# Kernel optimization log

Hardware: AMD Instinct MI355X
Metric: run time of the kernel (lower is better)

Reference implementation:

```python
import jax, jax.numpy as jnp
import numpy as np

B, N, D = 8, 2048, 512

def setup_inputs() -> dict:
    key = jax.random.key(0)
    k1, k2, k3, k4 = jax.random.split(key, 4)
    x = jax.random.normal(k1, (B, N, D), dtype=jnp.float32)
    x2 = jax.random.normal(k2, (B, N, D), dtype=jnp.float32)
    # nn.Linear(dim, dim): weight [D, D], bias [D]
    W = jax.random.normal(k3, (D, D), dtype=jnp.float32) * (1.0 / np.sqrt(D))
    b = jax.random.normal(k4, (D,), dtype=jnp.float32) * 0.01
    return {"x": x, "x2": x2, "W": W, "b": b}

def reference(x, x2, W, b):
    # key = softmax(x2.transpose(1,2), dim=1) -> softmax over feature axis D,
    # shape [B, D, N]; equivalently softmax(x2, axis=-1) then transpose.
    key_t = jax.nn.softmax(x2, axis=-1)          # [B, N, D], softmax over D
    query = jax.nn.softmax(x2, axis=1)            # [B, N, D], softmax over N
    # context = value @ key : [B,N,D] @ [B,D,N] -> [B,N,N]
    context = jnp.einsum('bnd,bmd->bnm', x, key_t)
    # atten = context @ query : [B,N,N] @ [B,N,D] -> [B,N,D]
    atten = jnp.einsum('bnm,bmd->bnd', context, query)
    # linear projection: atten @ W.T + b
    return jnp.einsum('bnd,ed->bne', atten, W) + b
```

## Files before the change

### kernel.cpp

```cpp
#include <hip/hip_runtime.h>


typedef __attribute__((ext_vector_type(8))) short          s16x8;
typedef __attribute__((ext_vector_type(8))) unsigned short u16x8;
typedef __attribute__((ext_vector_type(4))) float          f32x4;

#define B_ 8
#define N_ 2048
#define D_ 512

__device__ inline unsigned short f2bf(float f) {
    unsigned u = __float_as_uint(f);
    u += 0x7FFFu + ((u >> 16) & 1u);
    return (unsigned short)(u >> 16);
}

__global__ __launch_bounds__(256) void softmax_fused_k(const float* __restrict__ x2,
                                                       unsigned short* __restrict__ Ft,
                                                       float* __restrict__ qs) {
    __shared__ unsigned short ft[64][522];
    __shared__ float cp[4][512];
    int b = blockIdx.y, m0 = blockIdx.x * 64;
    int w = threadIdx.x >> 6, l = threadIdx.x & 63;
    const int c0 = l * 8;
    float colacc[8] = {0.f, 0.f, 0.f, 0.f, 0.f, 0.f, 0.f, 0.f};
#pragma unroll
    for (int it = 0; it < 16; ++it) {
        int row = w * 16 + it;
        const float* p = x2 + ((size_t)b * N_ + m0 + row) * D_ + c0;
        float4 a = *(const float4*)p;
        float4 bb = *(const float4*)(p + 4);
        float e0 = __expf(a.x), e1 = __expf(a.y), e2 = __expf(a.z), e3 = __expf(a.w);
        float e4 = __expf(bb.x), e5 = __expf(bb.y), e6 = __expf(bb.z), e7 = __expf(bb.w);
        float s = e0 + e1 + e2 + e3 + e4 + e5 + e6 + e7;
#pragma unroll
        for (int off = 1; off < 64; off <<= 1) s += __shfl_xor(s, off);
        float rv = rsqrtf(s);
        u16x8 o;
        o[0] = f2bf(e0 * rv); o[1] = f2bf(e1 * rv); o[2] = f2bf(e2 * rv); o[3] = f2bf(e3 * rv);
        o[4] = f2bf(e4 * rv); o[5] = f2bf(e5 * rv); o[6] = f2bf(e6 * rv); o[7] = f2bf(e7 * rv);
        *(u16x8*)&ft[row][c0] = o;
        colacc[0] += e0; colacc[1] += e1; colacc[2] += e2; colacc[3] += e3;
        colacc[4] += e4; colacc[5] += e5; colacc[6] += e6; colacc[7] += e7;
    }
#pragma unroll
    for (int c = 0; c < 8; ++c) cp[w][c0 + c] = colacc[c];
    __syncthreads();
    for (int c = threadIdx.x; c < 512; c += 256) {
        float s = cp[0][c] + cp[1][c] + cp[2][c] + cp[3][c];
        atomicAdd(&qs[b * D_ + c], s);
    }
#pragma unroll
    for (int half = 0; half < 2; ++half) {
        int d = threadIdx.x + half * 256;
        unsigned short* dst = Ft + ((size_t)b * D_ + d) * N_ + m0;
#pragma unroll
        for (int mv = 0; mv < 8; ++mv) {
            u16x8 o;
#pragma unroll
            for (int k = 0; k < 8; ++k) o[k] = ft[mv * 8 + k][d];
            *(u16x8*)(dst + mv * 8) = o;
        }
    }
}

__global__ __launch_bounds__(256) void cvt_bf16_k(const float* __restrict__ in,
                                                  unsigned short* __restrict__ out) {
    size_t i = ((size_t)blockIdx.x * 256 + threadIdx.x) * 8;
    float4 a = *(const float4*)(in + i);
    float4 b = *(const float4*)(in + i + 4);
    u16x8 o;
    o[0] = f2bf(a.x); o[1] = f2bf(a.y); o[2] = f2bf(a.z); o[3] = f2bf(a.w);
    o[4] = f2bf(b.x); o[5] = f2bf(b.y); o[6] = f2bf(b.z); o[7] = f2bf(b.w);
    *(u16x8*)(out + i) = o;
}

__global__ __launch_bounds__(256) void cvt_kq_k(const float* __restrict__ P,
                                                const float* __restrict__ qs,
                                                unsigned short* __restrict__ KQb) {
    size_t o = ((size_t)blockIdx.x * 256 + threadIdx.x) * 8;
    int b = (int)(o >> 18);
    size_t off = o & 262143;
    int j0 = (int)(o & 511);
    const float* base = P + (size_t)b * 4 * 262144 + off;
    float4 s0 = {0.f, 0.f, 0.f, 0.f}, s1 = {0.f, 0.f, 0.f, 0.f};
#pragma unroll
    for (int s = 0; s < 4; ++s) {
        float4 a0 = *(const float4*)(base + (size_t)s * 262144);
        float4 a1 = *(const float4*)(base + (size_t)s * 262144 + 4);
        s0.x += a0.x; s0.y += a0.y; s0.z += a0.z; s0.w += a0.w;
        s1.x += a1.x; s1.y += a1.y; s1.z += a1.z; s1.w += a1.w;
    }
    float4 q0 = *(const float4*)(qs + b * D_ + j0);
    float4 q1 = *(const float4*)(qs + b * D_ + j0 + 4);
    u16x8 r;
    r[0] = f2bf(s0.x / q0.x); r[1] = f2bf(s0.y / q0.y);
    r[2] = f2bf(s0.z / q0.z); r[3] = f2bf(s0.w / q0.w);
    r[4] = f2bf(s1.x / q1.x); r[5] = f2bf(s1.y / q1.y);
    r[6] = f2bf(s1.z / q1.z); r[7] = f2bf(s1.w / q1.w);
    *(u16x8*)(KQb + o) = r;
}

__device__ inline void gload16(const unsigned short* g, unsigned short* l) {
    __builtin_amdgcn_global_load_lds((const __attribute__((address_space(1))) void*)g,
                                     (__attribute__((address_space(3))) void*)l, 16, 0, 0);
}
__device__ inline void gload16f(const float* g, float* l) {
    __builtin_amdgcn_global_load_lds((const __attribute__((address_space(1))) void*)g,
                                     (__attribute__((address_space(3))) void*)l, 16, 0, 0);
}

__global__ __launch_bounds__(256, 2) void gemm128_p2_k(const unsigned short* __restrict__ Ft,
                                                       float* __restrict__ P) {
    __shared__ unsigned short As[128 * 32], Bs[128 * 32];
    const int nsplit = 4, K = N_;
    int z = blockIdx.z, b = z >> 2, ks = z & 3;
    int klen = K / nsplit, k0 = ks * klen;
    const unsigned short* Ab = Ft + (size_t)b * ((size_t)D_ * N_);
    int tid = threadIdx.x, w = tid >> 6, l = tid & 63;
    int wr = w >> 1, wc = w & 1;
    int lr = l & 15, lg = l >> 4;

    f32x4 acc[4][4];
#pragma unroll
    for (int i = 0; i < 4; ++i)
#pragma unroll
        for (int j = 0; j < 4; ++j) acc[i][j] = (f32x4){0.f, 0.f, 0.f, 0.f};

    const int rowbase = blockIdx.y * 128, colbase = blockIdx.x * 128;

    for (int kt = k0; kt < k0 + klen; kt += 32) {
#pragma unroll
        for (int i = 0; i < 2; ++i) {
            int ci = (i * 4 + w) * 64 + l;
            int row = ci >> 2, cc = ci & 3;
            gload16(Ab + (size_t)(rowbase + row) * K + kt + cc * 8, As + (i * 4 + w) * 512);
            gload16(Ab + (size_t)(colbase + row) * K + kt + cc * 8, Bs + (i * 4 + w) * 512);
        }
        __syncthreads();
        s16x8 af[4], bf[4];
#pragma unroll
        for (int i = 0; i < 4; ++i)
            af[i] = *(const s16x8*)&As[(wr * 64 + i * 16 + lr) * 32 + lg * 8];
#pragma unroll
        for (int j = 0; j < 4; ++j)
            bf[j] = *(const s16x8*)&Bs[(wc * 64 + j * 16 + lr) * 32 + lg * 8];
#pragma unroll
        for (int i = 0; i < 4; ++i)
#pragma unroll
            for (int j = 0; j < 4; ++j)
                acc[i][j] = __builtin_amdgcn_mfma_f32_16x16x32_bf16(af[i], bf[j], acc[i][j], 0, 0, 0);
        __syncthreads();
    }

    float* C = P + (size_t)z * 262144;
#pragma unroll
    for (int i = 0; i < 4; ++i)
#pragma unroll
        for (int j = 0; j < 4; ++j) {
            int col = colbase + wc * 64 + j * 16 + lr;
#pragma unroll
            for (int r = 0; r < 4; ++r) {
                int row = rowbase + wr * 64 + i * 16 + lg * 4 + r;
                C[(size_t)row * D_ + col] = acc[i][j][r];
            }
        }
}

__global__ __launch_bounds__(256, 4) void gemm64_k(const unsigned short* __restrict__ A,
                                                   const unsigned short* __restrict__ Bm,
                                                   unsigned short* __restrict__ Cv,
                                                   int K, long long sA, long long sB, long long sC) {
    __shared__ unsigned short As[64 * 32], Bs[64 * 32];
    int b = blockIdx.z;
    const unsigned short* Ab = A + (size_t)b * sA;
    const unsigned short* Bb = Bm + (size_t)b * sB;
    int tid = threadIdx.x, w = tid >> 6, l = tid & 63;
    int wr = w >> 1, wc = w & 1;
    int lr = l & 15, lg = l >> 4;
    int srow = tid >> 2, scc = tid & 3;

    f32x4 acc[2][2];
#pragma unroll
    for (int i = 0; i < 2; ++i)
#pragma unroll
        for (int j = 0; j < 2; ++j) acc[i][j] = (f32x4){0.f, 0.f, 0.f, 0.f};

    const int rowbase = blockIdx.y * 64, colbase = blockIdx.x * 64;

    for (int kt = 0; kt < K; kt += 32) {
        gload16(Ab + (size_t)(rowbase + srow) * K + kt + scc * 8, As + w * 512);
        gload16(Bb + (size_t)(colbase + srow) * K + kt + scc * 8, Bs + w * 512);
        __syncthreads();
        s16x8 af[2], bf[2];
#pragma unroll
        for (int i = 0; i < 2; ++i)
            af[i] = *(const s16x8*)&As[(wr * 32 + i * 16 + lr) * 32 + lg * 8];
#pragma unroll
        for (int j = 0; j < 2; ++j)
            bf[j] = *(const s16x8*)&Bs[(wc * 32 + j * 16 + lr) * 32 + lg * 8];
#pragma unroll
        for (int i = 0; i < 2; ++i)
#pragma unroll
            for (int j = 0; j < 2; ++j)
                acc[i][j] = __builtin_amdgcn_mfma_f32_16x16x32_bf16(af[i], bf[j], acc[i][j], 0, 0, 0);
        __syncthreads();
    }

    unsigned short* C = Cv + (size_t)b * sC;
#pragma unroll
    for (int i = 0; i < 2; ++i)
#pragma unroll
        for (int j = 0; j < 2; ++j) {
            int col = colbase + wc * 32 + j * 16 + lr;
#pragma unroll
            for (int r = 0; r < 4; ++r) {
                int row = rowbase + wr * 32 + i * 16 + lg * 4 + r;
                C[(size_t)row * D_ + col] = f2bf(acc[i][j][r]);
            }
        }
}

__global__ __launch_bounds__(256, 2) void gemm_xf32_k(const float* __restrict__ X,
                                                      const unsigned short* __restrict__ Bm,
                                                      float* __restrict__ Out,
                                                      const float* __restrict__ bias) {
    __shared__ float Asf[128 * 32];
    __shared__ unsigned short Bs[128 * 32];
    int b = blockIdx.z;
    const float* Ab = X + (size_t)b * ((size_t)N_ * D_);
    const unsigned short* Bb = Bm + (size_t)b * ((size_t)D_ * D_);
    int tm = blockIdx.y, tn = blockIdx.x;
    int tid = threadIdx.x, w = tid >> 6, l = tid & 63;
    int wr = w >> 1, wc = w & 1;
    int lr = l & 15, lg = l >> 4;

    f32x4 acc[4][4];
#pragma unroll
    for (int i = 0; i < 4; ++i)
#pragma unroll
        for (int j = 0; j < 4; ++j) acc[i][j] = (f32x4){0.f, 0.f, 0.f, 0.f};

    const int rowbase = tm * 128, colbase = tn * 128;

    for (int kt = 0; kt < D_; kt += 32) {
#pragma unroll
        for (int i = 0; i < 4; ++i) {
            int ci = (i * 4 + w) * 64 + l;
            int row = ci >> 3, cc = ci & 7;
            gload16f(Ab + (size_t)(rowbase + row) * D_ + kt + cc * 4, Asf + (i * 4 + w) * 256);
        }
#pragma unroll
        for (int i = 0; i < 2; ++i) {
            int ci = (i * 4 + w) * 64 + l;
            int row = ci >> 2, cc = ci & 3;
            gload16(Bb + (size_t)(colbase + row) * D_ + kt + cc * 8, Bs + (i * 4 + w) * 512);
        }
        __syncthreads();
        s16x8 af[4], bf[4];
#pragma unroll
        for (int i = 0; i < 4; ++i) {
            const float* ap = &Asf[(wr * 64 + i * 16 + lr) * 32 + lg * 8];
            f32x4 a0 = *(const f32x4*)ap, a1 = *(const f32x4*)(ap + 4);
            s16x8 t;
            t[0] = (short)f2bf(a0[0]); t[1] = (short)f2bf(a0[1]);
            t[2] = (short)f2bf(a0[2]); t[3] = (short)f2bf(a0[3]);
            t[4] = (short)f2bf(a1[0]); t[5] = (short)f2bf(a1[1]);
            t[6] = (short)f2bf(a1[2]); t[7] = (short)f2bf(a1[3]);
            af[i] = t;
        }
#pragma unroll
        for (int j = 0; j < 4; ++j)
            bf[j] = *(const s16x8*)&Bs[(wc * 64 + j * 16 + lr) * 32 + lg * 8];
#pragma unroll
        for (int i = 0; i < 4; ++i)
#pragma unroll
            for (int j = 0; j < 4; ++j)
                acc[i][j] = __builtin_amdgcn_mfma_f32_16x16x32_bf16(af[i], bf[j], acc[i][j], 0, 0, 0);
        __syncthreads();
    }

    float* C = Out + (size_t)b * ((size_t)N_ * D_);
#pragma unroll
    for (int i = 0; i < 4; ++i)
#pragma unroll
        for (int j = 0; j < 4; ++j) {
            int col = colbase + wc * 64 + j * 16 + lr;
            float bv = bias[col];
#pragma unroll
            for (int r = 0; r < 4; ++r) {
                int row = rowbase + wr * 64 + i * 16 + lg * 4 + r;
                C[(size_t)row * D_ + col] = acc[i][j][r] + bv;
            }
        }
}

extern "C" void kernel_launch(void* const* d_in, const int* in_sizes, int n_in,
                              void* d_out, int out_size, void* d_ws, size_t ws_size,
                              hipStream_t stream) {
    const float* x    = (const float*)d_in[0];
    const float* x2   = (const float*)d_in[1];
    const float* W    = (const float*)d_in[2];
    const float* bias = (const float*)d_in[3];
    float* out = (float*)d_out;

    unsigned short* Ft  = (unsigned short*)d_ws;
    unsigned short* Wb  = Ft + 8388608;
    unsigned short* KQb = Wb + 262144;
    unsigned short* Mt  = KQb + 2097152;
    float* P   = (float*)(Mt + 2097152);
    float* qs  = P + 8388608;

    hipMemsetAsync(qs, 0, (size_t)B_ * D_ * sizeof(float), stream);

    softmax_fused_k<<<dim3(N_ / 64, B_), 256, 0, stream>>>(x2, Ft, qs);

    cvt_bf16_k<<<dim3(128), 256, 0, stream>>>(W, Wb);

    gemm128_p2_k<<<dim3(4, 4, B_ * 4), 256, 0, stream>>>(Ft, P);

    cvt_kq_k<<<dim3(1024), 256, 0, stream>>>(P, qs, KQb);

    gemm64_k<<<dim3(8, 8, B_), 256, 0, stream>>>(
        Wb, KQb, Mt, 512, 0LL, (long long)512 * 512, (long long)512 * 512);

    gemm_xf32_k<<<dim3(4, 16, B_), 256, 0, stream>>>(x, Mt, out, bias);
}
```

Baseline: 174.4 us.

## Exploit symmetry of Gram GEMM, store split-K partials as bf16, shrink softmax tiles

The F^T F Gram matrix is symmetric, so the split-K GEMM now computes only the 10 upper-triangular 128x128 tiles per batch/split. The reduction kernel reads the lower triangle transposed. Partials are stored in bf16 instead of fp32 to halve the write and read traffic. The softmax kernel processes 32 rows per block for more blocks, and its transpose store becomes scalar 16-bit writes. The risks are extra rounding in the partial sums, uncoalesced strided reads for the mirrored tiles, and narrower Ft stores.

```diff
diff --git a/kernel.cpp b/kernel.cpp
--- a/kernel.cpp
+++ b/kernel.cpp
@@ -14,19 +14,22 @@
     u += 0x7FFFu + ((u >> 16) & 1u);
     return (unsigned short)(u >> 16);
 }
+__device__ inline float bf2f(unsigned short u) {
+    return __uint_as_float((unsigned)u << 16);
+}
 
 __global__ __launch_bounds__(256) void softmax_fused_k(const float* __restrict__ x2,
                                                        unsigned short* __restrict__ Ft,
                                                        float* __restrict__ qs) {
-    __shared__ unsigned short ft[64][522];
+    __shared__ unsigned short ft[32][522];
     __shared__ float cp[4][512];
-    int b = blockIdx.y, m0 = blockIdx.x * 64;
+    int b = blockIdx.y, m0 = blockIdx.x * 32;
     int w = threadIdx.x >> 6, l = threadIdx.x & 63;
     const int c0 = l * 8;
     float colacc[8] = {0.f, 0.f, 0.f, 0.f, 0.f, 0.f, 0.f, 0.f};
 #pragma unroll
-    for (int it = 0; it < 16; ++it) {
-        int row = w * 16 + it;
+    for (int it = 0; it < 8; ++it) {
+        int row = w * 8 + it;
         const float* p = x2 + ((size_t)b * N_ + m0 + row) * D_ + c0;
         float4 a = *(const float4*)p;
         float4 bb = *(const float4*)(p + 4);
@@ -50,17 +53,11 @@
         float s = cp[0][c] + cp[1][c] + cp[2][c] + cp[3][c];
         atomicAdd(&qs[b * D_ + c], s);
     }
-#pragma unroll
-    for (int half = 0; half < 2; ++half) {
-        int d = threadIdx.x + half * 256;
-        unsigned short* dst = Ft + ((size_t)b * D_ + d) * N_ + m0;
-#pragma unroll
-        for (int mv = 0; mv < 8; ++mv) {
-            u16x8 o;
-#pragma unroll
-            for (int k = 0; k < 8; ++k) o[k] = ft[mv * 8 + k][d];
-            *(u16x8*)(dst + mv * 8) = o;
-        }
+    int md = threadIdx.x & 31, dd = threadIdx.x >> 5;
+#pragma unroll
+    for (int di = 0; di < 64; ++di) {
+        int d = di * 8 + dd;
+        Ft[((size_t)b * D_ + d) * N_ + m0 + md] = ft[md][d];
     }
 }
 
@@ -75,29 +72,41 @@
     *(u16x8*)(out + i) = o;
 }
 
-__global__ __launch_bounds__(256) void cvt_kq_k(const float* __restrict__ P,
+__global__ __launch_bounds__(256) void cvt_kq_k(const unsigned short* __restrict__ Pbf,
                                                 const float* __restrict__ qs,
                                                 unsigned short* __restrict__ KQb) {
     size_t o = ((size_t)blockIdx.x * 256 + threadIdx.x) * 8;
     int b = (int)(o >> 18);
     size_t off = o & 262143;
-    int j0 = (int)(o & 511);
-    const float* base = P + (size_t)b * 4 * 262144 + off;
-    float4 s0 = {0.f, 0.f, 0.f, 0.f}, s1 = {0.f, 0.f, 0.f, 0.f};
-#pragma unroll
-    for (int s = 0; s < 4; ++s) {
-        float4 a0 = *(const float4*)(base + (size_t)s * 262144);
-        float4 a1 = *(const float4*)(base + (size_t)s * 262144 + 4);
-        s0.x += a0.x; s0.y += a0.y; s0.z += a0.z; s0.w += a0.w;
-        s1.x += a1.x; s1.y += a1.y; s1.z += a1.z; s1.w += a1.w;
+    int i = (int)(off >> 9);
+    int j0 = (int)(off & 511);
+    const unsigned short* Pb = Pbf + (size_t)b * 4 * 262144;
+    float sm[8] = {0.f, 0.f, 0.f, 0.f, 0.f, 0.f, 0.f, 0.f};
+    if ((i >> 7) <= (j0 >> 7)) {
+        const unsigned short* p = Pb + (size_t)i * 512 + j0;
+#pragma unroll
+        for (int s = 0; s < 4; ++s) {
+            u16x8 v = *(const u16x8*)(p + (size_t)s * 262144);
+#pragma unroll
+            for (int k = 0; k < 8; ++k) sm[k] += bf2f(v[k]);
+        }
+    } else {
+#pragma unroll
+        for (int k = 0; k < 8; ++k) {
+            float acc = 0.f;
+#pragma unroll
+            for (int s = 0; s < 4; ++s)
+                acc += bf2f(Pb[(size_t)s * 262144 + (size_t)(j0 + k) * 512 + i]);
+            sm[k] = acc;
+        }
     }
     float4 q0 = *(const float4*)(qs + b * D_ + j0);
     float4 q1 = *(const float4*)(qs + b * D_ + j0 + 4);
     u16x8 r;
-    r[0] = f2bf(s0.x / q0.x); r[1] = f2bf(s0.y / q0.y);
-    r[2] = f2bf(s0.z / q0.z); r[3] = f2bf(s0.w / q0.w);
-    r[4] = f2bf(s1.x / q1.x); r[5] = f2bf(s1.y / q1.y);
-    r[6] = f2bf(s1.z / q1.z); r[7] = f2bf(s1.w / q1.w);
+    r[0] = f2bf(sm[0] / q0.x); r[1] = f2bf(sm[1] / q0.y);
+    r[2] = f2bf(sm[2] / q0.z); r[3] = f2bf(sm[3] / q0.w);
+    r[4] = f2bf(sm[4] / q1.x); r[5] = f2bf(sm[5] / q1.y);
+    r[6] = f2bf(sm[6] / q1.z); r[7] = f2bf(sm[7] / q1.w);
     *(u16x8*)(KQb + o) = r;
 }
 
@@ -111,11 +120,13 @@
 }
 
 __global__ __launch_bounds__(256, 2) void gemm128_p2_k(const unsigned short* __restrict__ Ft,
-                                                       float* __restrict__ P) {
+                                                       unsigned short* __restrict__ Pbf) {
     __shared__ unsigned short As[128 * 32], Bs[128 * 32];
-    const int nsplit = 4, K = N_;
-    int z = blockIdx.z, b = z >> 2, ks = z & 3;
-    int klen = K / nsplit, k0 = ks * klen;
+    int t = blockIdx.x;
+    int ty = (t < 4) ? 0 : (t < 7) ? 1 : (t < 9) ? 2 : 3;
+    int tx = t - ((ty == 0) ? 0 : (ty == 1) ? 3 : (ty == 2) ? 5 : 6);
+    int z = blockIdx.y, b = z >> 2, ks = z & 3;
+    int k0 = ks * 512;
     const unsigned short* Ab = Ft + (size_t)b * ((size_t)D_ * N_);
     int tid = threadIdx.x, w = tid >> 6, l = tid & 63;
     int wr = w >> 1, wc = w & 1;
@@ -127,15 +138,15 @@
 #pragma unroll
         for (int j = 0; j < 4; ++j) acc[i][j] = (f32x4){0.f, 0.f, 0.f, 0.f};
 
-    const int rowbase = blockIdx.y * 128, colbase = blockIdx.x * 128;
-
-    for (int kt = k0; kt < k0 + klen; kt += 32) {
+    const int rowbase = ty * 128, colbase = tx * 128;
+
+    for (int kt = k0; kt < k0 + 512; kt += 32) {
 #pragma unroll
         for (int i = 0; i < 2; ++i) {
             int ci = (i * 4 + w) * 64 + l;
             int row = ci >> 2, cc = ci & 3;
-            gload16(Ab + (size_t)(rowbase + row) * K + kt + cc * 8, As + (i * 4 + w) * 512);
-            gload16(Ab + (size_t)(colbase + row) * K + kt + cc * 8, Bs + (i * 4 + w) * 512);
+            gload16(Ab + (size_t)(rowbase + row) * N_ + kt + cc * 8, As + (i * 4 + w) * 512);
+            gload16(Ab + (size_t)(colbase + row) * N_ + kt + cc * 8, Bs + (i * 4 + w) * 512);
         }
         __syncthreads();
         s16x8 af[4], bf[4];
@@ -153,7 +164,7 @@
         __syncthreads();
     }
 
-    float* C = P + (size_t)z * 262144;
+    unsigned short* C = Pbf + (size_t)z * 262144;
 #pragma unroll
     for (int i = 0; i < 4; ++i)
 #pragma unroll
@@ -162,7 +173,7 @@
 #pragma unroll
             for (int r = 0; r < 4; ++r) {
                 int row = rowbase + wr * 64 + i * 16 + lg * 4 + r;
-                C[(size_t)row * D_ + col] = acc[i][j][r];
+                C[(size_t)row * 512 + col] = f2bf(acc[i][j][r]);
             }
         }
 }
@@ -308,18 +319,18 @@
     unsigned short* Wb  = Ft + 8388608;
     unsigned short* KQb = Wb + 262144;
     unsigned short* Mt  = KQb + 2097152;
-    float* P   = (float*)(Mt + 2097152);
-    float* qs  = P + 8388608;
+    unsigned short* Pbf = Mt + 2097152;
+    float* qs = (float*)(Pbf + 8388608);
 
     hipMemsetAsync(qs, 0, (size_t)B_ * D_ * sizeof(float), stream);
 
-    softmax_fused_k<<<dim3(N_ / 64, B_), 256, 0, stream>>>(x2, Ft, qs);
+    softmax_fused_k<<<dim3(N_ / 32, B_), 256, 0, stream>>>(x2, Ft, qs);
 
     cvt_bf16_k<<<dim3(128), 256, 0, stream>>>(W, Wb);
 
-    gemm128_p2_k<<<dim3(4, 4, B_ * 4), 256, 0, stream>>>(Ft, P);
-
-    cvt_kq_k<<<dim3(1024), 256, 0, stream>>>(P, qs, KQb);
+    gemm128_p2_k<<<dim3(10, 32), 256, 0, stream>>>(Ft, Pbf);
+
+    cvt_kq_k<<<dim3(1024), 256, 0, stream>>>(Pbf, qs, KQb);
 
     gemm64_k<<<dim3(8, 8, B_), 256, 0, stream>>>(
         Wb, KQb, Mt, 512, 0LL, (long long)512 * 512, (long long)512 * 512);
```

Result: slower. 183.1 us (+5.0%).
